# Kernel optimization log

Hardware: AMD Instinct MI355X
Metric: run time of the kernel (lower is better)

The kernel has to match this reference:

```python
import jax, jax.numpy as jnp
import numpy as np

K_OUTLIER = 16   # decomposition_topk default k
Q = 127.0        # int8 symmetric quant scale


def _quantize(mat):
    # per-row abs-max symmetric quantization; torch .to(int8) truncates toward
    # zero, which matches XLA's float->int convert semantics.
    mmax = jnp.max(jnp.abs(mat), axis=-1)                      # [...,]
    q = (mat * (Q / mmax)[..., None]).astype(jnp.int8)
    return q, mmax


def setup_inputs() -> dict:
    key = jax.random.key(0)
    k1, k2, k3 = jax.random.split(key, 3)
    B, I, O = 4096, 2048, 2048
    x = jax.random.normal(k1, (B, I), jnp.float32)
    weight = jax.random.normal(k2, (O, I), jnp.float32) * 0.02  # nn.Linear convention [out, in]
    bias = jax.random.normal(k3, (O,), jnp.float32) * 0.02
    return {"x": x, "weight": weight, "bias": bias}


def reference(x, weight, bias):
    # --- weight-side prep (done once in __init__ in the torch module) ---
    col_max = jnp.max(jnp.abs(weight), axis=0)                 # [I] abs-max per input column
    idx = jax.lax.top_k(col_max, K_OUTLIER)[1]                 # [k] outlier input columns
    w_unq = weight[:, idx].T                                   # [k, O] fp outlier weights
    w0 = weight.at[:, idx].set(0.0)                            # zero outlier columns
    w_q, w_max = _quantize(w0)                                 # int8 [O, I], fp [O]

    # --- activation side ---
    x_unq = x[:, idx]                                          # [B, k]
    x1 = x.at[:, idx].set(0.0)
    x_q, x_max = _quantize(x1)                                 # int8 [B, I], fp [B]

    # int8 matmul accumulated in int32 (MatMulInteger), then dequantize
    res_q_i32 = jnp.matmul(x_q.astype(jnp.int32), w_q.T.astype(jnp.int32))  # [B, O]
    mx = x_max[:, None] * w_max[None, :]                       # outer product of row/col maxes
    res_q = (res_q_i32.astype(jnp.float32) / (Q * Q)).astype(jnp.float16).astype(jnp.float32) * mx

    # fp outlier path + bias
    res_unq = x_unq @ w_unq + bias                             # [B, O]
    return res_q + res_unq
```

## Files before the change

kernel.cpp:

```cpp
#include <hip/hip_runtime.h>
#include <hip/hip_fp16.h>
#include <stdint.h>

#define I_DIM 2048
#define O_DIM 2048
#define B_DIM 4096
#define KOUT 16

typedef int i32x4 __attribute__((ext_vector_type(4)));
typedef float f32x4 __attribute__((ext_vector_type(4)));
typedef _Float16 f16x8 __attribute__((ext_vector_type(8)));

#define TO_LDS(p) ((__attribute__((address_space(3))) void*)(p))
#define TO_GLB(p) ((const __attribute__((address_space(1))) void*)(p))

__global__ void colmax_kernel(const float* __restrict__ W, unsigned* __restrict__ cm) {
  int j = blockIdx.x * 256 + threadIdx.x;
  int i0 = blockIdx.y * 64;
  float m = 0.0f;
  const float* p = W + (size_t)i0 * I_DIM + j;
  for (int i = 0; i < 64; ++i)
    m = fmaxf(m, fabsf(p[(size_t)i * I_DIM]));
  atomicMax(cm + j, __float_as_uint(m));
}

__global__ void topk_kernel(const unsigned* __restrict__ cm, int* __restrict__ idx,
                            float* __restrict__ keep) {
  int t = threadIdx.x;
  const float4* c4 = (const float4*)cm;
  float4 a = c4[t * 2], b = c4[t * 2 + 1];
  float v[8] = {a.x, a.y, a.z, a.w, b.x, b.y, b.z, b.w};
  for (int j = t; j < I_DIM; j += 256) keep[j] = 1.0f;
  __shared__ float wm_[4];
  __shared__ int wi_[4];
  __shared__ int sel;
  for (int k = 0; k < KOUT; ++k) {
    float m = v[0]; int mi = 0;
#pragma unroll
    for (int r = 1; r < 8; ++r) if (v[r] > m) { m = v[r]; mi = r; }
    int gi = t * 8 + mi;
#pragma unroll
    for (int s = 32; s; s >>= 1) {
      float om = __shfl_down(m, s);
      int oi = __shfl_down(gi, s);
      if (om > m) { m = om; gi = oi; }
    }
    if ((t & 63) == 0) { wm_[t >> 6] = m; wi_[t >> 6] = gi; }
    __syncthreads();
    if (t == 0) {
      float bm = wm_[0]; int bi = wi_[0];
      for (int w2 = 1; w2 < 4; ++w2) if (wm_[w2] > bm) { bm = wm_[w2]; bi = wi_[w2]; }
      idx[k] = bi; keep[bi] = 0.0f; sel = bi;
    }
    __syncthreads();
    if (t == (sel >> 3)) v[sel & 7] = -1.0f;
  }
}

__global__ __launch_bounds__(256) void quant_kernel(
    const float* __restrict__ X, const float* __restrict__ W,
    const float* __restrict__ keep, const int* __restrict__ idx,
    signed char* __restrict__ xq, signed char* __restrict__ wq,
    float* __restrict__ xmax, float* __restrict__ wmax,
    _Float16* __restrict__ xunqh,
    _Float16* __restrict__ wunqh) {
  int b = blockIdx.x;
  int t = threadIdx.x;
  bool isW = b < O_DIM;
  int r = isW ? b : (b - O_DIM);
  const float* src = isW ? (W + (size_t)r * I_DIM) : (X + (size_t)r * I_DIM);
  const float4* s4 = (const float4*)src;
  const float4* k4 = (const float4*)keep;
  float4 v0 = s4[t], v1 = s4[t + 256];
  float4 k0 = k4[t], k1 = k4[t + 256];
  v0.x *= k0.x; v0.y *= k0.y; v0.z *= k0.z; v0.w *= k0.w;
  v1.x *= k1.x; v1.y *= k1.y; v1.z *= k1.z; v1.w *= k1.w;
  float m = fmaxf(fmaxf(fmaxf(fabsf(v0.x), fabsf(v0.y)), fmaxf(fabsf(v0.z), fabsf(v0.w))),
                  fmaxf(fmaxf(fabsf(v1.x), fabsf(v1.y)), fmaxf(fabsf(v1.z), fabsf(v1.w))));
#pragma unroll
  for (int s = 32; s; s >>= 1) m = fmaxf(m, __shfl_xor(m, s));
  __shared__ float red[4];
  if ((t & 63) == 0) red[t >> 6] = m;
  __syncthreads();
  m = fmaxf(fmaxf(red[0], red[1]), fmaxf(red[2], red[3]));
  float sc = 127.0f / m;
  unsigned p0 = (unsigned char)(signed char)(int)(v0.x * sc)
              | ((unsigned)(unsigned char)(signed char)(int)(v0.y * sc) << 8)
              | ((unsigned)(unsigned char)(signed char)(int)(v0.z * sc) << 16)
              | ((unsigned)(unsigned char)(signed char)(int)(v0.w * sc) << 24);
  unsigned p1 = (unsigned char)(signed char)(int)(v1.x * sc)
              | ((unsigned)(unsigned char)(signed char)(int)(v1.y * sc) << 8)
              | ((unsigned)(unsigned char)(signed char)(int)(v1.z * sc) << 16)
              | ((unsigned)(unsigned char)(signed char)(int)(v1.w * sc) << 24);
  unsigned* qout = (unsigned*)(isW ? (wq + (size_t)r * I_DIM) : (xq + (size_t)r * I_DIM));
  qout[t] = p0;
  qout[t + 256] = p1;
  if (t == 0) { if (isW) wmax[r] = m; else xmax[r] = m; }
  if (t < KOUT) {
    float ov = src[idx[t]];
    _Float16* u = isW ? (wunqh + (size_t)r * 32) : (xunqh + (size_t)r * 32);
    u[t] = (_Float16)ov;
    u[t + KOUT] = (_Float16)0.0f;
  }
}

__global__ __launch_bounds__(256, 2) void gemm_kernel(
    const signed char* __restrict__ Aq,
    const signed char* __restrict__ Bq,
    const float* __restrict__ xmaxg,
    const float* __restrict__ wmaxg,
    const _Float16* __restrict__ xunqh,
    const _Float16* __restrict__ wunqh,
    const float* __restrict__ biasg,
    float* __restrict__ out) {
  constexpr int N = O_DIM, K = I_DIM;
  __shared__ __align__(16) signed char smem[2][32768];

  const int tid = threadIdx.x;
  const int lane = tid & 63;
  const int wave = tid >> 6;
  const int wm = (wave & 1) * 64;
  const int wn = (wave >> 1) * 64;

  const int lid = blockIdx.y * gridDim.x + blockIdx.x;
  const int xcd = lid & 7;
  const int pos = lid >> 3;
  const int by = (xcd >> 1) * 8 + (pos >> 3);
  const int bx = (xcd & 1) * 8 + (pos & 7);
  const int m0 = by * 128;
  const int n0 = bx * 128;

  const int srow = tid >> 3;
  const int cslot = tid & 7;
  const int fm = lane & 15;
  const int q = lane >> 4;

  i32x4 acc[4][4] = {};

  auto stage = [&](int buf, int kt) {
    signed char* As = &smem[buf][0];
    signed char* Bs = &smem[buf][16384];
#pragma unroll
    for (int a = 0; a < 4; ++a) {
      const int row = a * 32 + srow;
      const int gch = (cslot - (row >> 1)) & 7;
      const signed char* ga = Aq + (size_t)(m0 + row) * K + kt + gch * 16;
      const signed char* gb = Bq + (size_t)(n0 + row) * K + kt + gch * 16;
      __builtin_amdgcn_global_load_lds(TO_GLB(ga), TO_LDS(As + a * 4096 + tid * 16), 16, 0, 0);
      __builtin_amdgcn_global_load_lds(TO_GLB(gb), TO_LDS(Bs + a * 4096 + tid * 16), 16, 0, 0);
    }
  };

  stage(0, 0);
  __syncthreads();

#pragma unroll 2
  for (int t = 0; t < K / 128; ++t) {
    const int cur = t & 1;
    if (t < K / 128 - 1) stage(cur ^ 1, (t + 1) * 128);
    const signed char* As = &smem[cur][0];
    const signed char* Bs = &smem[cur][16384];
#pragma unroll
    for (int s = 0; s < 2; ++s) {
      i32x4 af[4], bf[4];
      const int q8 = s * 4 + q;
#pragma unroll
      for (int i = 0; i < 4; ++i) {
        const int ra = wm + i * 16 + fm;
        af[i] = *(const i32x4*)(As + ra * 128 + (((q8 + (ra >> 1)) & 7) << 4));
        const int rb = wn + i * 16 + fm;
        bf[i] = *(const i32x4*)(Bs + rb * 128 + (((q8 + (rb >> 1)) & 7) << 4));
      }
#pragma unroll
      for (int i = 0; i < 4; ++i)
#pragma unroll
        for (int j = 0; j < 4; ++j)
          acc[i][j] = __builtin_amdgcn_mfma_i32_16x16x64_i8(af[i], bf[j], acc[i][j], 0, 0, 0);
    }
    __syncthreads();
  }

  f16x8 afh[4], bfh[4];
#pragma unroll
  for (int i = 0; i < 4; ++i)
    afh[i] = *(const f16x8*)(xunqh + (size_t)(m0 + wm + i * 16 + fm) * 32 + q * 8);
#pragma unroll
  for (int j = 0; j < 4; ++j)
    bfh[j] = *(const f16x8*)(wunqh + (size_t)(n0 + wn + j * 16 + fm) * 32 + q * 8);

#pragma unroll
  for (int i = 0; i < 4; ++i) {
    f32x4 xmv = *(const f32x4*)(xmaxg + m0 + wm + i * 16 + q * 4);
#pragma unroll
    for (int j = 0; j < 4; ++j) {
      int cl = n0 + wn + j * 16 + fm;
      float wmv = wmaxg[cl];
      float bv = biasg[cl];
      f32x4 c;
#pragma unroll
      for (int r = 0; r < 4; ++r) {
        float v = (float)acc[i][j][r] / 16129.0f;
        v = __half2float(__float2half(v));
        c[r] = v * (xmv[r] * wmv) + bv;
      }
      c = __builtin_amdgcn_mfma_f32_16x16x32_f16(afh[i], bfh[j], c, 0, 0, 0);
#pragma unroll
      for (int r = 0; r < 4; ++r)
        out[(size_t)(m0 + wm + i * 16 + q * 4 + r) * N + cl] = c[r];
    }
  }
}

extern "C" void kernel_launch(void* const* d_in, const int* in_sizes, int n_in,
                              void* d_out, int out_size, void* d_ws, size_t ws_size,
                              hipStream_t stream) {
  const float* x    = (const float*)d_in[0];
  const float* w    = (const float*)d_in[1];
  const float* bias = (const float*)d_in[2];
  float* out = (float*)d_out;
  char* ws = (char*)d_ws;

  unsigned* cm     = (unsigned*)(ws + 0);
  int* idx         = (int*)(ws + 8192);
  float* keep      = (float*)(ws + 8320);
  float* w_max     = (float*)(ws + 16512);
  float* x_max     = (float*)(ws + 24704);
  _Float16* x_unqh = (_Float16*)(ws + 41088);
  _Float16* w_unqh = (_Float16*)(ws + 303232);
  signed char* w_q = (signed char*)(ws + 434304);
  signed char* x_q = (signed char*)(ws + 4628608);

  hipMemsetAsync(cm, 0, 8192, stream);
  colmax_kernel<<<dim3(8, 32), 256, 0, stream>>>(w, cm);
  topk_kernel<<<1, 256, 0, stream>>>(cm, idx, keep);
  quant_kernel<<<O_DIM + B_DIM, 256, 0, stream>>>(x, w, keep, idx, x_q, w_q,
                                                  x_max, w_max, x_unqh, w_unqh);
  gemm_kernel<<<dim3(O_DIM / 128, B_DIM / 128), 256, 0, stream>>>(
      x_q, w_q, x_max, w_max, x_unqh, w_unqh, bias, out);
}
```

Measured before the change: 144.9 us.

## Fuse colmax, topk, quant and GEMM into one persistent kernel with grid barriers

Merges the four kernels into a single 512-block persistent kernel that moves between phases through a software grid barrier built on atomics. This removes three kernel-launch gaps and their tail effects. In exchange, topk runs on one block while all the others spin, quant is limited to 512 resident blocks looping over rows, and the barrier depends on all 512 blocks being co-resident (two per CU at 64KB LDS). The spin loop has a timeout, so a block could proceed before the others arrive if that limit is hit.

```diff
diff --git a/kernel.cpp b/kernel.cpp
--- a/kernel.cpp
+++ b/kernel.cpp
@@ -6,6 +6,7 @@
 #define O_DIM 2048
 #define B_DIM 4096
 #define KOUT 16
+#define NBLK 512
 
 typedef int i32x4 __attribute__((ext_vector_type(4)));
 typedef float f32x4 __attribute__((ext_vector_type(4)));
@@ -14,199 +15,220 @@
 #define TO_LDS(p) ((__attribute__((address_space(3))) void*)(p))
 #define TO_GLB(p) ((const __attribute__((address_space(1))) void*)(p))
 
-__global__ void colmax_kernel(const float* __restrict__ W, unsigned* __restrict__ cm) {
-  int j = blockIdx.x * 256 + threadIdx.x;
-  int i0 = blockIdx.y * 64;
-  float m = 0.0f;
-  const float* p = W + (size_t)i0 * I_DIM + j;
-  for (int i = 0; i < 64; ++i)
-    m = fmaxf(m, fabsf(p[(size_t)i * I_DIM]));
-  atomicMax(cm + j, __float_as_uint(m));
+__device__ __forceinline__ void grid_barrier(unsigned* cnt, unsigned* gen) {
+  __syncthreads();
+  if (threadIdx.x == 0) {
+    __threadfence();
+    unsigned g = __hip_atomic_load(gen, __ATOMIC_RELAXED, __HIP_MEMORY_SCOPE_AGENT);
+    unsigned arrived = __hip_atomic_fetch_add(cnt, 1u, __ATOMIC_ACQ_REL, __HIP_MEMORY_SCOPE_AGENT);
+    if (arrived == NBLK - 1) {
+      __hip_atomic_store(cnt, 0u, __ATOMIC_RELAXED, __HIP_MEMORY_SCOPE_AGENT);
+      __hip_atomic_fetch_add(gen, 1u, __ATOMIC_RELEASE, __HIP_MEMORY_SCOPE_AGENT);
+    } else {
+      long spin = 0;
+      while (__hip_atomic_load(gen, __ATOMIC_ACQUIRE, __HIP_MEMORY_SCOPE_AGENT) == g) {
+        if (++spin > 40000000L) break;
+      }
+    }
+    __threadfence();
+  }
+  __syncthreads();
 }
 
-__global__ void topk_kernel(const unsigned* __restrict__ cm, int* __restrict__ idx,
-                            float* __restrict__ keep) {
-  int t = threadIdx.x;
-  const float4* c4 = (const float4*)cm;
-  float4 a = c4[t * 2], b = c4[t * 2 + 1];
-  float v[8] = {a.x, a.y, a.z, a.w, b.x, b.y, b.z, b.w};
-  for (int j = t; j < I_DIM; j += 256) keep[j] = 1.0f;
+__global__ __launch_bounds__(256, 2) void mega_kernel(
+    const float* __restrict__ X, const float* __restrict__ W,
+    const float* __restrict__ biasg,
+    unsigned* __restrict__ cm, unsigned* __restrict__ bar,
+    int* __restrict__ idx, float* __restrict__ keep,
+    signed char* __restrict__ xq, signed char* __restrict__ wq,
+    float* __restrict__ xmax, float* __restrict__ wmax,
+    _Float16* __restrict__ xunqh,
+    _Float16* __restrict__ wunqh,
+    float* __restrict__ out) {
+  __shared__ __align__(16) signed char smem[2][32768];
   __shared__ float wm_[4];
   __shared__ int wi_[4];
   __shared__ int sel;
-  for (int k = 0; k < KOUT; ++k) {
-    float m = v[0]; int mi = 0;
-#pragma unroll
-    for (int r = 1; r < 8; ++r) if (v[r] > m) { m = v[r]; mi = r; }
-    int gi = t * 8 + mi;
-#pragma unroll
-    for (int s = 32; s; s >>= 1) {
-      float om = __shfl_down(m, s);
-      int oi = __shfl_down(gi, s);
-      if (om > m) { m = om; gi = oi; }
-    }
-    if ((t & 63) == 0) { wm_[t >> 6] = m; wi_[t >> 6] = gi; }
+
+  const int tid = threadIdx.x;
+  const int bid = blockIdx.x;
+  unsigned* bcnt = bar;
+  unsigned* bgen = bar + 1;
+
+  {
+    const int cb = bid & 7;
+    const int rc = bid >> 3;
+    const int j = cb * 256 + tid;
+    const float* p = W + (size_t)(rc * 32) * I_DIM + j;
+    float m = 0.0f;
+#pragma unroll 8
+    for (int i = 0; i < 32; ++i)
+      m = fmaxf(m, fabsf(p[(size_t)i * I_DIM]));
+    atomicMax(cm + j, __float_as_uint(m));
+  }
+  grid_barrier(bcnt, bgen);
+
+  if (bid == 0) {
+    const float4* c4 = (const float4*)cm;
+    float4 a = c4[tid * 2], b = c4[tid * 2 + 1];
+    float v[8] = {a.x, a.y, a.z, a.w, b.x, b.y, b.z, b.w};
+    for (int j = tid; j < I_DIM; j += 256) keep[j] = 1.0f;
+    for (int k = 0; k < KOUT; ++k) {
+      float m = v[0]; int mi = 0;
+#pragma unroll
+      for (int r = 1; r < 8; ++r) if (v[r] > m) { m = v[r]; mi = r; }
+      int gi = tid * 8 + mi;
+#pragma unroll
+      for (int s = 32; s; s >>= 1) {
+        float om = __shfl_down(m, s);
+        int oi = __shfl_down(gi, s);
+        if (om > m) { m = om; gi = oi; }
+      }
+      if ((tid & 63) == 0) { wm_[tid >> 6] = m; wi_[tid >> 6] = gi; }
+      __syncthreads();
+      if (tid == 0) {
+        float bm = wm_[0]; int bi = wi_[0];
+        for (int w2 = 1; w2 < 4; ++w2) if (wm_[w2] > bm) { bm = wm_[w2]; bi = wi_[w2]; }
+        idx[k] = bi; keep[bi] = 0.0f; sel = bi;
+      }
+      __syncthreads();
+      if (tid == (sel >> 3)) v[sel & 7] = -1.0f;
+    }
+  }
+  grid_barrier(bcnt, bgen);
+
+  for (int u = bid; u < O_DIM + B_DIM; u += NBLK) {
+    bool isW = u < O_DIM;
+    int r = isW ? u : (u - O_DIM);
+    const float* src = isW ? (W + (size_t)r * I_DIM) : (X + (size_t)r * I_DIM);
+    const float4* s4 = (const float4*)src;
+    const float4* k4 = (const float4*)keep;
+    float4 v0 = s4[tid], v1 = s4[tid + 256];
+    float4 k0 = k4[tid], k1 = k4[tid + 256];
+    v0.x *= k0.x; v0.y *= k0.y; v0.z *= k0.z; v0.w *= k0.w;
+    v1.x *= k1.x; v1.y *= k1.y; v1.z *= k1.z; v1.w *= k1.w;
+    float m = fmaxf(fmaxf(fmaxf(fabsf(v0.x), fabsf(v0.y)), fmaxf(fabsf(v0.z), fabsf(v0.w))),
+                    fmaxf(fmaxf(fabsf(v1.x), fabsf(v1.y)), fmaxf(fabsf(v1.z), fabsf(v1.w))));
+#pragma unroll
+    for (int s = 32; s; s >>= 1) m = fmaxf(m, __shfl_xor(m, s));
+    if ((tid & 63) == 0) wm_[tid >> 6] = m;
     __syncthreads();
-    if (t == 0) {
-      float bm = wm_[0]; int bi = wi_[0];
-      for (int w2 = 1; w2 < 4; ++w2) if (wm_[w2] > bm) { bm = wm_[w2]; bi = wi_[w2]; }
-      idx[k] = bi; keep[bi] = 0.0f; sel = bi;
+    m = fmaxf(fmaxf(wm_[0], wm_[1]), fmaxf(wm_[2], wm_[3]));
+    float sc = 127.0f / m;
+    unsigned p0 = (unsigned char)(signed char)(int)(v0.x * sc)
+                | ((unsigned)(unsigned char)(signed char)(int)(v0.y * sc) << 8)
+                | ((unsigned)(unsigned char)(signed char)(int)(v0.z * sc) << 16)
+                | ((unsigned)(unsigned char)(signed char)(int)(v0.w * sc) << 24);
+    unsigned p1 = (unsigned char)(signed char)(int)(v1.x * sc)
+                | ((unsigned)(unsigned char)(signed char)(int)(v1.y * sc) << 8)
+                | ((unsigned)(unsigned char)(signed char)(int)(v1.z * sc) << 16)
+                | ((unsigned)(unsigned char)(signed char)(int)(v1.w * sc) << 24);
+    unsigned* qout = (unsigned*)(isW ? (wq + (size_t)r * I_DIM) : (xq + (size_t)r * I_DIM));
+    qout[tid] = p0;
+    qout[tid + 256] = p1;
+    if (tid == 0) { if (isW) wmax[r] = m; else xmax[r] = m; }
+    if (tid < KOUT) {
+      float ov = src[idx[tid]];
+      _Float16* u16 = isW ? (wunqh + (size_t)r * 32) : (xunqh + (size_t)r * 32);
+      u16[tid] = (_Float16)ov;
+      u16[tid + KOUT] = (_Float16)0.0f;
     }
     __syncthreads();
-    if (t == (sel >> 3)) v[sel & 7] = -1.0f;
-  }
-}
-
-__global__ __launch_bounds__(256) void quant_kernel(
-    const float* __restrict__ X, const float* __restrict__ W,
-    const float* __restrict__ keep, const int* __restrict__ idx,
-    signed char* __restrict__ xq, signed char* __restrict__ wq,
-    float* __restrict__ xmax, float* __restrict__ wmax,
-    _Float16* __restrict__ xunqh,
-    _Float16* __restrict__ wunqh) {
-  int b = blockIdx.x;
-  int t = threadIdx.x;
-  bool isW = b < O_DIM;
-  int r = isW ? b : (b - O_DIM);
-  const float* src = isW ? (W + (size_t)r * I_DIM) : (X + (size_t)r * I_DIM);
-  const float4* s4 = (const float4*)src;
-  const float4* k4 = (const float4*)keep;
-  float4 v0 = s4[t], v1 = s4[t + 256];
-  float4 k0 = k4[t], k1 = k4[t + 256];
-  v0.x *= k0.x; v0.y *= k0.y; v0.z *= k0.z; v0.w *= k0.w;
-  v1.x *= k1.x; v1.y *= k1.y; v1.z *= k1.z; v1.w *= k1.w;
-  float m = fmaxf(fmaxf(fmaxf(fabsf(v0.x), fabsf(v0.y)), fmaxf(fabsf(v0.z), fabsf(v0.w))),
-                  fmaxf(fmaxf(fabsf(v1.x), fabsf(v1.y)), fmaxf(fabsf(v1.z), fabsf(v1.w))));
-#pragma unroll
-  for (int s = 32; s; s >>= 1) m = fmaxf(m, __shfl_xor(m, s));
-  __shared__ float red[4];
-  if ((t & 63) == 0) red[t >> 6] = m;
-  __syncthreads();
-  m = fmaxf(fmaxf(red[0], red[1]), fmaxf(red[2], red[3]));
-  float sc = 127.0f / m;
-  unsigned p0 = (unsigned char)(signed char)(int)(v0.x * sc)
-              | ((unsigned)(unsigned char)(signed char)(int)(v0.y * sc) << 8)
-              | ((unsigned)(unsigned char)(signed char)(int)(v0.z * sc) << 16)
-              | ((unsigned)(unsigned char)(signed char)(int)(v0.w * sc) << 24);
-  unsigned p1 = (unsigned char)(signed char)(int)(v1.x * sc)
-              | ((unsigned)(unsigned char)(signed char)(int)(v1.y * sc) << 8)
-              | ((unsigned)(unsigned char)(signed char)(int)(v1.z * sc) << 16)
-              | ((unsigned)(unsigned char)(signed char)(int)(v1.w * sc) << 24);
-  unsigned* qout = (unsigned*)(isW ? (wq + (size_t)r * I_DIM) : (xq + (size_t)r * I_DIM));
-  qout[t] = p0;
-  qout[t + 256] = p1;
-  if (t == 0) { if (isW) wmax[r] = m; else xmax[r] = m; }
-  if (t < KOUT) {
-    float ov = src[idx[t]];
-    _Float16* u = isW ? (wunqh + (size_t)r * 32) : (xunqh + (size_t)r * 32);
-    u[t] = (_Float16)ov;
-    u[t + KOUT] = (_Float16)0.0f;
-  }
-}
-
-__global__ __launch_bounds__(256, 2) void gemm_kernel(
-    const signed char* __restrict__ Aq,
-    const signed char* __restrict__ Bq,
-    const float* __restrict__ xmaxg,
-    const float* __restrict__ wmaxg,
-    const _Float16* __restrict__ xunqh,
-    const _Float16* __restrict__ wunqh,
-    const float* __restrict__ biasg,
-    float* __restrict__ out) {
-  constexpr int N = O_DIM, K = I_DIM;
-  __shared__ __align__(16) signed char smem[2][32768];
-
-  const int tid = threadIdx.x;
-  const int lane = tid & 63;
-  const int wave = tid >> 6;
-  const int wm = (wave & 1) * 64;
-  const int wn = (wave >> 1) * 64;
-
-  const int lid = blockIdx.y * gridDim.x + blockIdx.x;
-  const int xcd = lid & 7;
-  const int pos = lid >> 3;
-  const int by = (xcd >> 1) * 8 + (pos >> 3);
-  const int bx = (xcd & 1) * 8 + (pos & 7);
-  const int m0 = by * 128;
-  const int n0 = bx * 128;
-
-  const int srow = tid >> 3;
-  const int cslot = tid & 7;
-  const int fm = lane & 15;
-  const int q = lane >> 4;
-
-  i32x4 acc[4][4] = {};
-
-  auto stage = [&](int buf, int kt) {
-    signed char* As = &smem[buf][0];
-    signed char* Bs = &smem[buf][16384];
-#pragma unroll
-    for (int a = 0; a < 4; ++a) {
-      const int row = a * 32 + srow;
-      const int gch = (cslot - (row >> 1)) & 7;
-      const signed char* ga = Aq + (size_t)(m0 + row) * K + kt + gch * 16;
-      const signed char* gb = Bq + (size_t)(n0 + row) * K + kt + gch * 16;
-      __builtin_amdgcn_global_load_lds(TO_GLB(ga), TO_LDS(As + a * 4096 + tid * 16), 16, 0, 0);
-      __builtin_amdgcn_global_load_lds(TO_GLB(gb), TO_LDS(Bs + a * 4096 + tid * 16), 16, 0, 0);
-    }
-  };
-
-  stage(0, 0);
-  __syncthreads();
+  }
+  grid_barrier(bcnt, bgen);
+
+  {
+    constexpr int N = O_DIM, K = I_DIM;
+    const int lane = tid & 63;
+    const int wave = tid >> 6;
+    const int wm = (wave & 1) * 64;
+    const int wn = (wave >> 1) * 64;
+
+    const int xcd = bid & 7;
+    const int pos = bid >> 3;
+    const int by = (xcd >> 1) * 8 + (pos >> 3);
+    const int bx = (xcd & 1) * 8 + (pos & 7);
+    const int m0 = by * 128;
+    const int n0 = bx * 128;
+
+    const int srow = tid >> 3;
+    const int cslot = tid & 7;
+    const int fm = lane & 15;
+    const int q = lane >> 4;
+
+    i32x4 acc[4][4] = {};
+
+    auto stage = [&](int buf, int kt) {
+      signed char* As = &smem[buf][0];
+      signed char* Bs = &smem[buf][16384];
+#pragma unroll
+      for (int a = 0; a < 4; ++a) {
+        const int row = a * 32 + srow;
+        const int gch = (cslot - (row >> 1)) & 7;
+        const signed char* ga = xq + (size_t)(m0 + row) * K + kt + gch * 16;
+        const signed char* gb = wq + (size_t)(n0 + row) * K + kt + gch * 16;
+        __builtin_amdgcn_global_load_lds(TO_GLB(ga), TO_LDS(As + a * 4096 + tid * 16), 16, 0, 0);
+        __builtin_amdgcn_global_load_lds(TO_GLB(gb), TO_LDS(Bs + a * 4096 + tid * 16), 16, 0, 0);
+      }
+    };
+
+    stage(0, 0);
+    __syncthreads();
 
 #pragma unroll 2
-  for (int t = 0; t < K / 128; ++t) {
-    const int cur = t & 1;
-    if (t < K / 128 - 1) stage(cur ^ 1, (t + 1) * 128);
-    const signed char* As = &smem[cur][0];
-    const signed char* Bs = &smem[cur][16384];
-#pragma unroll
-    for (int s = 0; s < 2; ++s) {
-      i32x4 af[4], bf[4];
-      const int q8 = s * 4 + q;
-#pragma unroll
-      for (int i = 0; i < 4; ++i) {
-        const int ra = wm + i * 16 + fm;
-        af[i] = *(const i32x4*)(As + ra * 128 + (((q8 + (ra >> 1)) & 7) << 4));
-        const int rb = wn + i * 16 + fm;
-        bf[i] = *(const i32x4*)(Bs + rb * 128 + (((q8 + (rb >> 1)) & 7) << 4));
-      }
-#pragma unroll
-      for (int i = 0; i < 4; ++i)
-#pragma unroll
-        for (int j = 0; j < 4; ++j)
-          acc[i][j] = __builtin_amdgcn_mfma_i32_16x16x64_i8(af[i], bf[j], acc[i][j], 0, 0, 0);
-    }
-    __syncthreads();
-  }
-
-  f16x8 afh[4], bfh[4];
-#pragma unroll
-  for (int i = 0; i < 4; ++i)
-    afh[i] = *(const f16x8*)(xunqh + (size_t)(m0 + wm + i * 16 + fm) * 32 + q * 8);
-#pragma unroll
-  for (int j = 0; j < 4; ++j)
-    bfh[j] = *(const f16x8*)(wunqh + (size_t)(n0 + wn + j * 16 + fm) * 32 + q * 8);
-
-#pragma unroll
-  for (int i = 0; i < 4; ++i) {
-    f32x4 xmv = *(const f32x4*)(xmaxg + m0 + wm + i * 16 + q * 4);
-#pragma unroll
-    for (int j = 0; j < 4; ++j) {
-      int cl = n0 + wn + j * 16 + fm;
-      float wmv = wmaxg[cl];
-      float bv = biasg[cl];
-      f32x4 c;
-#pragma unroll
-      for (int r = 0; r < 4; ++r) {
-        float v = (float)acc[i][j][r] / 16129.0f;
-        v = __half2float(__float2half(v));
-        c[r] = v * (xmv[r] * wmv) + bv;
-      }
-      c = __builtin_amdgcn_mfma_f32_16x16x32_f16(afh[i], bfh[j], c, 0, 0, 0);
-#pragma unroll
-      for (int r = 0; r < 4; ++r)
-        out[(size_t)(m0 + wm + i * 16 + q * 4 + r) * N + cl] = c[r];
+    for (int t = 0; t < K / 128; ++t) {
+      const int cur = t & 1;
+      if (t < K / 128 - 1) stage(cur ^ 1, (t + 1) * 128);
+      const signed char* As = &smem[cur][0];
+      const signed char* Bs = &smem[cur][16384];
+#pragma unroll
+      for (int s = 0; s < 2; ++s) {
+        i32x4 af[4], bf[4];
+        const int q8 = s * 4 + q;
+#pragma unroll
+        for (int i = 0; i < 4; ++i) {
+          const int ra = wm + i * 16 + fm;
+          af[i] = *(const i32x4*)(As + ra * 128 + (((q8 + (ra >> 1)) & 7) << 4));
+          const int rb = wn + i * 16 + fm;
+          bf[i] = *(const i32x4*)(Bs + rb * 128 + (((q8 + (rb >> 1)) & 7) << 4));
+        }
+#pragma unroll
+        for (int i = 0; i < 4; ++i)
+#pragma unroll
+          for (int j = 0; j < 4; ++j)
+            acc[i][j] = __builtin_amdgcn_mfma_i32_16x16x64_i8(af[i], bf[j], acc[i][j], 0, 0, 0);
+      }
+      __syncthreads();
+    }
+
+    f16x8 afh[4], bfh[4];
+#pragma unroll
+    for (int i = 0; i < 4; ++i)
+      afh[i] = *(const f16x8*)(xunqh + (size_t)(m0 + wm + i * 16 + fm) * 32 + q * 8);
+#pragma unroll
+    for (int j = 0; j < 4; ++j)
+      bfh[j] = *(const f16x8*)(wunqh + (size_t)(n0 + wn + j * 16 + fm) * 32 + q * 8);
+
+#pragma unroll
+    for (int i = 0; i < 4; ++i) {
+      f32x4 xmv = *(const f32x4*)(xmax + m0 + wm + i * 16 + q * 4);
+#pragma unroll
+      for (int j = 0; j < 4; ++j) {
+        int cl = n0 + wn + j * 16 + fm;
+        float wmv = wmax[cl];
+        float bv = biasg[cl];
+        f32x4 c;
+#pragma unroll
+        for (int r = 0; r < 4; ++r) {
+          float v = (float)acc[i][j][r] / 16129.0f;
+          v = __half2float(__float2half(v));
+          c[r] = v * (xmv[r] * wmv) + bv;
+        }
+        c = __builtin_amdgcn_mfma_f32_16x16x32_f16(afh[i], bfh[j], c, 0, 0, 0);
+#pragma unroll
+        for (int r = 0; r < 4; ++r)
+          out[(size_t)(m0 + wm + i * 16 + q * 4 + r) * N + cl] = c[r];
+      }
     }
   }
 }
@@ -221,20 +243,19 @@
   char* ws = (char*)d_ws;
 
   unsigned* cm     = (unsigned*)(ws + 0);
-  int* idx         = (int*)(ws + 8192);
-  float* keep      = (float*)(ws + 8320);
-  float* w_max     = (float*)(ws + 16512);
-  float* x_max     = (float*)(ws + 24704);
-  _Float16* x_unqh = (_Float16*)(ws + 41088);
-  _Float16* w_unqh = (_Float16*)(ws + 303232);
-  signed char* w_q = (signed char*)(ws + 434304);
-  signed char* x_q = (signed char*)(ws + 4628608);
-
-  hipMemsetAsync(cm, 0, 8192, stream);
-  colmax_kernel<<<dim3(8, 32), 256, 0, stream>>>(w, cm);
-  topk_kernel<<<1, 256, 0, stream>>>(cm, idx, keep);
-  quant_kernel<<<O_DIM + B_DIM, 256, 0, stream>>>(x, w, keep, idx, x_q, w_q,
-                                                  x_max, w_max, x_unqh, w_unqh);
-  gemm_kernel<<<dim3(O_DIM / 128, B_DIM / 128), 256, 0, stream>>>(
-      x_q, w_q, x_max, w_max, x_unqh, w_unqh, bias, out);
+  unsigned* bar    = (unsigned*)(ws + 8192);
+  int* idx         = (int*)(ws + 8320);
+  float* keep      = (float*)(ws + 8448);
+  float* w_max     = (float*)(ws + 16640);
+  float* x_max     = (float*)(ws + 24832);
+  _Float16* x_unqh = (_Float16*)(ws + 41216);
+  _Float16* w_unqh = (_Float16*)(ws + 303360);
+  signed char* w_q = (signed char*)(ws + 434432);
+  signed char* x_q = (signed char*)(ws + 4628736);
+
+  hipMemsetAsync(ws, 0, 8256, stream);
+
+  mega_kernel<<<dim3(NBLK), dim3(256), 0, stream>>>(
+      x, w, bias, cm, bar, idx, keep, x_q, w_q, x_max, w_max,
+      x_unqh, w_unqh, out);
 }
```

New measurement: 335.2 us. +131.3%, slower.

## Fuse top-k selection into quantization kernel and process one row per wave

Applied to the files above, without the earlier changes.

Removes the separate single-block top-k kernel launch by having every block of the quantization kernel recompute the top-16 outlier columns redundantly into shared memory. Quantization now assigns one row per wave, 12 rows per block, using a wave-level shuffle reduction with no block-level barrier. The column-max kernel also gets twice as many blocks with shorter loops. The trade is that the serial top-k loop, with its 32 barriers, is repeated in all 512 blocks rather than run once.

```diff
diff --git a/kernel.cpp b/kernel.cpp
--- a/kernel.cpp
+++ b/kernel.cpp
@@ -16,24 +16,38 @@
 
 __global__ void colmax_kernel(const float* __restrict__ W, unsigned* __restrict__ cm) {
   int j = blockIdx.x * 256 + threadIdx.x;
-  int i0 = blockIdx.y * 64;
+  int i0 = blockIdx.y * 32;
   float m = 0.0f;
   const float* p = W + (size_t)i0 * I_DIM + j;
-  for (int i = 0; i < 64; ++i)
+#pragma unroll 8
+  for (int i = 0; i < 32; ++i)
     m = fmaxf(m, fabsf(p[(size_t)i * I_DIM]));
   atomicMax(cm + j, __float_as_uint(m));
 }
 
-__global__ void topk_kernel(const unsigned* __restrict__ cm, int* __restrict__ idx,
-                            float* __restrict__ keep) {
-  int t = threadIdx.x;
+__global__ __launch_bounds__(256) void quant_topk_kernel(
+    const float* __restrict__ X, const float* __restrict__ W,
+    const unsigned* __restrict__ cm,
+    signed char* __restrict__ xq, signed char* __restrict__ wq,
+    float* __restrict__ xmax, float* __restrict__ wmax,
+    _Float16* __restrict__ xunqh,
+    _Float16* __restrict__ wunqh) {
+  __shared__ float keepL[I_DIM];
+  __shared__ int idxL[KOUT];
+  __shared__ float wm_[4];
+  __shared__ int wi_[4];
+  __shared__ int sel;
+
+  const int t = threadIdx.x;
+
   const float4* c4 = (const float4*)cm;
   float4 a = c4[t * 2], b = c4[t * 2 + 1];
   float v[8] = {a.x, a.y, a.z, a.w, b.x, b.y, b.z, b.w};
-  for (int j = t; j < I_DIM; j += 256) keep[j] = 1.0f;
-  __shared__ float wm_[4];
-  __shared__ int wi_[4];
-  __shared__ int sel;
+  {
+    float4 one = {1.0f, 1.0f, 1.0f, 1.0f};
+    ((float4*)keepL)[t] = one;
+    ((float4*)keepL)[t + 256] = one;
+  }
   for (int k = 0; k < KOUT; ++k) {
     float m = v[0]; int mi = 0;
 #pragma unroll
@@ -50,57 +64,53 @@
     if (t == 0) {
       float bm = wm_[0]; int bi = wi_[0];
       for (int w2 = 1; w2 < 4; ++w2) if (wm_[w2] > bm) { bm = wm_[w2]; bi = wi_[w2]; }
-      idx[k] = bi; keep[bi] = 0.0f; sel = bi;
+      idxL[k] = bi; keepL[bi] = 0.0f; sel = bi;
     }
     __syncthreads();
     if (t == (sel >> 3)) v[sel & 7] = -1.0f;
   }
-}
-
-__global__ __launch_bounds__(256) void quant_kernel(
-    const float* __restrict__ X, const float* __restrict__ W,
-    const float* __restrict__ keep, const int* __restrict__ idx,
-    signed char* __restrict__ xq, signed char* __restrict__ wq,
-    float* __restrict__ xmax, float* __restrict__ wmax,
-    _Float16* __restrict__ xunqh,
-    _Float16* __restrict__ wunqh) {
-  int b = blockIdx.x;
-  int t = threadIdx.x;
-  bool isW = b < O_DIM;
-  int r = isW ? b : (b - O_DIM);
-  const float* src = isW ? (W + (size_t)r * I_DIM) : (X + (size_t)r * I_DIM);
-  const float4* s4 = (const float4*)src;
-  const float4* k4 = (const float4*)keep;
-  float4 v0 = s4[t], v1 = s4[t + 256];
-  float4 k0 = k4[t], k1 = k4[t + 256];
-  v0.x *= k0.x; v0.y *= k0.y; v0.z *= k0.z; v0.w *= k0.w;
-  v1.x *= k1.x; v1.y *= k1.y; v1.z *= k1.z; v1.w *= k1.w;
-  float m = fmaxf(fmaxf(fmaxf(fabsf(v0.x), fabsf(v0.y)), fmaxf(fabsf(v0.z), fabsf(v0.w))),
-                  fmaxf(fmaxf(fabsf(v1.x), fabsf(v1.y)), fmaxf(fabsf(v1.z), fabsf(v1.w))));
-#pragma unroll
-  for (int s = 32; s; s >>= 1) m = fmaxf(m, __shfl_xor(m, s));
-  __shared__ float red[4];
-  if ((t & 63) == 0) red[t >> 6] = m;
   __syncthreads();
-  m = fmaxf(fmaxf(red[0], red[1]), fmaxf(red[2], red[3]));
-  float sc = 127.0f / m;
-  unsigned p0 = (unsigned char)(signed char)(int)(v0.x * sc)
-              | ((unsigned)(unsigned char)(signed char)(int)(v0.y * sc) << 8)
-              | ((unsigned)(unsigned char)(signed char)(int)(v0.z * sc) << 16)
-              | ((unsigned)(unsigned char)(signed char)(int)(v0.w * sc) << 24);
-  unsigned p1 = (unsigned char)(signed char)(int)(v1.x * sc)
-              | ((unsigned)(unsigned char)(signed char)(int)(v1.y * sc) << 8)
-              | ((unsigned)(unsigned char)(signed char)(int)(v1.z * sc) << 16)
-              | ((unsigned)(unsigned char)(signed char)(int)(v1.w * sc) << 24);
-  unsigned* qout = (unsigned*)(isW ? (wq + (size_t)r * I_DIM) : (xq + (size_t)r * I_DIM));
-  qout[t] = p0;
-  qout[t + 256] = p1;
-  if (t == 0) { if (isW) wmax[r] = m; else xmax[r] = m; }
-  if (t < KOUT) {
-    float ov = src[idx[t]];
-    _Float16* u = isW ? (wunqh + (size_t)r * 32) : (xunqh + (size_t)r * 32);
-    u[t] = (_Float16)ov;
-    u[t + KOUT] = (_Float16)0.0f;
+
+  const int wave = t >> 6;
+  const int lane = t & 63;
+  for (int rr = wave; rr < 12; rr += 4) {
+    const int u = blockIdx.x * 12 + rr;
+    const bool isW = u < O_DIM;
+    const int r = isW ? u : (u - O_DIM);
+    const float* src = isW ? (W + (size_t)r * I_DIM) : (X + (size_t)r * I_DIM);
+    const float4* s4 = (const float4*)src;
+    const float4* k4 = (const float4*)keepL;
+
+    float4 d[8];
+    float mx = 0.0f;
+#pragma unroll
+    for (int i = 0; i < 8; ++i) {
+      float4 dv = s4[i * 64 + lane];
+      float4 kk = k4[i * 64 + lane];
+      dv.x *= kk.x; dv.y *= kk.y; dv.z *= kk.z; dv.w *= kk.w;
+      d[i] = dv;
+      mx = fmaxf(mx, fmaxf(fmaxf(fabsf(dv.x), fabsf(dv.y)),
+                           fmaxf(fabsf(dv.z), fabsf(dv.w))));
+    }
+#pragma unroll
+    for (int s = 32; s; s >>= 1) mx = fmaxf(mx, __shfl_xor(mx, s));
+    const float sc = 127.0f / mx;
+    unsigned* qout = (unsigned*)(isW ? (wq + (size_t)r * I_DIM) : (xq + (size_t)r * I_DIM));
+#pragma unroll
+    for (int i = 0; i < 8; ++i) {
+      unsigned p = (unsigned char)(signed char)(int)(d[i].x * sc)
+                 | ((unsigned)(unsigned char)(signed char)(int)(d[i].y * sc) << 8)
+                 | ((unsigned)(unsigned char)(signed char)(int)(d[i].z * sc) << 16)
+                 | ((unsigned)(unsigned char)(signed char)(int)(d[i].w * sc) << 24);
+      qout[i * 64 + lane] = p;
+    }
+    if (lane == 0) { if (isW) wmax[r] = mx; else xmax[r] = mx; }
+    if (lane < KOUT) {
+      float ov = src[idxL[lane]];
+      _Float16* u16 = isW ? (wunqh + (size_t)r * 32) : (xunqh + (size_t)r * 32);
+      u16[lane] = (_Float16)ov;
+      u16[lane + KOUT] = (_Float16)0.0f;
+    }
   }
 }
 
@@ -221,20 +231,17 @@
   char* ws = (char*)d_ws;
 
   unsigned* cm     = (unsigned*)(ws + 0);
-  int* idx         = (int*)(ws + 8192);
-  float* keep      = (float*)(ws + 8320);
-  float* w_max     = (float*)(ws + 16512);
-  float* x_max     = (float*)(ws + 24704);
-  _Float16* x_unqh = (_Float16*)(ws + 41088);
-  _Float16* w_unqh = (_Float16*)(ws + 303232);
-  signed char* w_q = (signed char*)(ws + 434304);
-  signed char* x_q = (signed char*)(ws + 4628608);
+  float* w_max     = (float*)(ws + 8192);
+  float* x_max     = (float*)(ws + 16384);
+  _Float16* x_unqh = (_Float16*)(ws + 32768);
+  _Float16* w_unqh = (_Float16*)(ws + 294912);
+  signed char* w_q = (signed char*)(ws + 425984);
+  signed char* x_q = (signed char*)(ws + 4620288);
 
   hipMemsetAsync(cm, 0, 8192, stream);
-  colmax_kernel<<<dim3(8, 32), 256, 0, stream>>>(w, cm);
-  topk_kernel<<<1, 256, 0, stream>>>(cm, idx, keep);
-  quant_kernel<<<O_DIM + B_DIM, 256, 0, stream>>>(x, w, keep, idx, x_q, w_q,
-                                                  x_max, w_max, x_unqh, w_unqh);
+  colmax_kernel<<<dim3(8, 64), 256, 0, stream>>>(w, cm);
+  quant_topk_kernel<<<512, 256, 0, stream>>>(x, w, cm, x_q, w_q,
+                                             x_max, w_max, x_unqh, w_unqh);
   gemm_kernel<<<dim3(O_DIM / 128, B_DIM / 128), 256, 0, stream>>>(
       x_q, w_q, x_max, w_max, x_unqh, w_unqh, bias, out);
 }
```

Measured after the change: 138.5 us. 4.4% less time.
